# Performance work log

Measured on AMD Instinct MI355X. Metric: run time of the kernel, lower is better.

## Reference

```python
import jax, jax.numpy as jnp
import numpy as np

N_NAMED = 8000   # len(e_dict)
ANON_E = 192     # cfg.anon_e
EMB_DIM = 128    # cfg.emb_dim
N_CLASS = 100
N_REL = 50


def setup_inputs() -> dict:
    key = jax.random.key(0)
    ks = jax.random.split(key, 6)
    s = 1.0 / np.sqrt(EMB_DIM)  # xavier-ish scale
    return {
        "anon_e_emb": jax.random.normal(ks[0], (ANON_E, EMB_DIM), dtype=jnp.float32) * s,
        "e_table": jax.random.normal(ks[1], (N_NAMED, EMB_DIM), dtype=jnp.float32) * s,
        "c_table": jax.random.normal(ks[2], (N_CLASS, EMB_DIM), dtype=jnp.float32) * s,
        "r_table": jax.random.normal(ks[3], (N_REL, EMB_DIM), dtype=jnp.float32) * s,
        "fc0_w": jax.random.normal(ks[4], (1, 2 * EMB_DIM), dtype=jnp.float32) * s,
        "fc0_b": jnp.zeros((1,), dtype=jnp.float32),
        "c_id": 7,
        "r_id": 3,
    }


def reference(anon_e_emb, e_table, c_table, r_table, fc0_w, fc0_b, c_id, r_id):
    """FALCON forward for axiom ObjectSomeValuesFrom(<r> <c>), product t-norm.

    Faithful to _get_c_fs, _get_r_fs, _logical_exist:
      c_fs[j]   = sigmoid(fc_0([c_emb ; e_j]))
      r_fs[i,j] = sigmoid(fc_0([e_i + r_emb ; e_j]))
      out[i]    = max_j r_fs[i,j] * c_fs[j]
    fc_0(cat([l, r])) = l @ w_l + r @ w_r + b  (Linear(2d -> 1)), so the
    [N, N, 2d] concat collapses to two [N] GEMVs plus a broadcast add.
    """
    d = e_table.shape[1]
    e_all = jnp.concatenate([e_table, anon_e_emb], axis=0)  # [N, d]
    w_l = fc0_w[0, :d]   # weights for the left (concat) half
    w_r = fc0_w[0, d:]   # weights for the right half
    b = fc0_b[0]

    c_emb = c_table[c_id]  # [d]
    r_emb = r_table[r_id]  # [d]

    # c_fs: fuzzy membership of every entity in class c  -> [N]
    c_fs = jax.nn.sigmoid(jnp.dot(c_emb, w_l) + e_all @ w_r + b)

    # r_fs[i, j] = sigmoid((e_i + r) . w_l + e_j . w_r + b)  -> [N, N]
    row = (e_all + r_emb) @ w_l  # [N]
    col = e_all @ w_r            # [N]
    r_fs = jax.nn.sigmoid(row[:, None] + col[None, :] + b)

    # _logical_exist with product t-norm: max_j (r_fs * c_fs)
    return jnp.max(r_fs * c_fs[None, :], axis=-1)  # [N]
```

## Files before the change

kernel.cpp:

```cpp
#include <hip/hip_runtime.h>


#define N_NAMED 8000
#define N_ALL   8192
#define D       128
#define K1_BLOCKS (N_ALL / 8)

__global__ __launch_bounds__(256) void k_dots(
    const float* __restrict__ anon_e, const float* __restrict__ e_table,
    const float* __restrict__ fc0_w, float* __restrict__ rowdot,
    float* __restrict__ colmax_part)
{
    const int tid = threadIdx.x;
    const int g   = tid >> 5;
    const int l   = tid & 31;
    const int row = blockIdx.x * 8 + g;

    const float4* rp = (row < N_NAMED)
        ? (const float4*)(e_table + (size_t)row * D)
        : (const float4*)(anon_e + (size_t)(row - N_NAMED) * D);

    float4 e  = rp[l];
    float4 wl = ((const float4*)fc0_w)[l];
    float4 wr = ((const float4*)fc0_w)[32 + l];

    float dl = e.x*wl.x + e.y*wl.y + e.z*wl.z + e.w*wl.w;
    float dr = e.x*wr.x + e.y*wr.y + e.z*wr.z + e.w*wr.w;

    #pragma unroll
    for (int off = 16; off >= 1; off >>= 1) {
        dl += __shfl_xor(dl, off, 64);
        dr += __shfl_xor(dr, off, 64);
    }

    __shared__ float scol[8];
    if (l == 0) { rowdot[row] = dl; scol[g] = dr; }
    __syncthreads();
    if (tid == 0) {
        float m = scol[0];
        #pragma unroll
        for (int i = 1; i < 8; i++) m = fmaxf(m, scol[i]);
        colmax_part[blockIdx.x] = m;
    }
}

__global__ __launch_bounds__(256) void k_final(
    const float* __restrict__ c_table, const float* __restrict__ r_table,
    const float* __restrict__ fc0_w, const float* __restrict__ fc0_b,
    const int* __restrict__ c_id, const int* __restrict__ r_id,
    const float* __restrict__ colmax_part, float* __restrict__ out)
{
    const int tid = threadIdx.x;
    const int i   = blockIdx.x * 256 + tid;

    float m = colmax_part[tid];
    m = fmaxf(m, colmax_part[tid + 256]);
    m = fmaxf(m, colmax_part[tid + 512]);
    m = fmaxf(m, colmax_part[tid + 768]);
    #pragma unroll
    for (int off = 32; off >= 1; off >>= 1)
        m = fmaxf(m, __shfl_xor(m, off, 64));

    __shared__ float swm[4];
    __shared__ float smax;
    if ((tid & 63) == 0) swm[tid >> 6] = m;
    __syncthreads();
    if (tid == 0)
        smax = fmaxf(fmaxf(swm[0], swm[1]), fmaxf(swm[2], swm[3]));
    __syncthreads();
    const float colmax = smax;

    const float b = fc0_b[0];
    const float* cp = c_table + (size_t)c_id[0] * D;
    const float* rp = r_table + (size_t)r_id[0] * D;
    float cw = 0.f, rw = 0.f;
    #pragma unroll 8
    for (int t = 0; t < D; t++) {
        float w = fc0_w[t];
        cw = fmaf(cp[t], w, cw);
        rw = fmaf(rp[t], w, rw);
    }

    float a1 = out[i] + rw + colmax + b;
    float a2 = cw + colmax + b;
    float s1 = 1.f / (1.f + __expf(-a1));
    float s2 = 1.f / (1.f + __expf(-a2));
    out[i] = s1 * s2;
}

extern "C" void kernel_launch(void* const* d_in, const int* in_sizes, int n_in,
                              void* d_out, int out_size, void* d_ws, size_t ws_size,
                              hipStream_t stream) {
    const float* anon_e  = (const float*)d_in[0];
    const float* e_table = (const float*)d_in[1];
    const float* c_table = (const float*)d_in[2];
    const float* r_table = (const float*)d_in[3];
    const float* fc0_w   = (const float*)d_in[4];
    const float* fc0_b   = (const float*)d_in[5];
    const int*   c_id    = (const int*)d_in[6];
    const int*   r_id    = (const int*)d_in[7];
    float* out = (float*)d_out;
    float* ws  = (float*)d_ws;

    k_dots<<<K1_BLOCKS, 256, 0, stream>>>(anon_e, e_table, fc0_w, out, ws);
    k_final<<<N_ALL / 256, 256, 0, stream>>>(c_table, r_table, fc0_w, fc0_b,
                                             c_id, r_id, ws, out);
}
```

Baseline: 75.72 us.

## Fuse dot and finalize kernels into one cooperative kernel with grid sync

Merges the two kernels into a single cooperative launch of 256 blocks, each handling 32 rows. Row dots stay in shared memory instead of a global round trip, and a grid-wide sync replaces the second kernel launch before the column max is reduced. The c/r dot products now use a vectorized warp reduction instead of a serial loop in every thread. The cost is the grid-barrier overhead, and the launch depends on all blocks being co-resident.

```diff
diff --git a/kernel.cpp b/kernel.cpp
--- a/kernel.cpp
+++ b/kernel.cpp
@@ -1,91 +1,92 @@
 #include <hip/hip_runtime.h>
+#include <hip/hip_cooperative_groups.h>
+
+namespace cg = cooperative_groups;
 
 
 #define N_NAMED 8000
 #define N_ALL   8192
 #define D       128
-#define K1_BLOCKS (N_ALL / 8)
+#define NBLK    256
+#define ROWS_PER_BLK (N_ALL / NBLK)
 
-__global__ __launch_bounds__(256) void k_dots(
+__global__ __launch_bounds__(256) void k_fused(
     const float* __restrict__ anon_e, const float* __restrict__ e_table,
-    const float* __restrict__ fc0_w, float* __restrict__ rowdot,
-    float* __restrict__ colmax_part)
+    const float* __restrict__ c_table, const float* __restrict__ r_table,
+    const float* __restrict__ fc0_w, const float* __restrict__ fc0_b,
+    const int* __restrict__ c_id, const int* __restrict__ r_id,
+    float* __restrict__ part, float* __restrict__ out)
 {
     const int tid = threadIdx.x;
     const int g   = tid >> 5;
     const int l   = tid & 31;
-    const int row = blockIdx.x * 8 + g;
 
-    const float4* rp = (row < N_NAMED)
-        ? (const float4*)(e_table + (size_t)row * D)
-        : (const float4*)(anon_e + (size_t)(row - N_NAMED) * D);
+    const float4 wl = ((const float4*)fc0_w)[l];
+    const float4 wr = ((const float4*)fc0_w)[32 + l];
 
-    float4 e  = rp[l];
-    float4 wl = ((const float4*)fc0_w)[l];
-    float4 wr = ((const float4*)fc0_w)[32 + l];
+    __shared__ float sdl[ROWS_PER_BLK];
+    __shared__ float sred[8];
+    __shared__ float swm[4];
+    __shared__ float s_cw, s_rw;
 
-    float dl = e.x*wl.x + e.y*wl.y + e.z*wl.z + e.w*wl.w;
-    float dr = e.x*wr.x + e.y*wr.y + e.z*wr.z + e.w*wr.w;
-
+    float dmax = -3.0e38f;
     #pragma unroll
-    for (int off = 16; off >= 1; off >>= 1) {
-        dl += __shfl_xor(dl, off, 64);
-        dr += __shfl_xor(dr, off, 64);
+    for (int p = 0; p < 4; p++) {
+        const int row = blockIdx.x * ROWS_PER_BLK + p * 8 + g;
+        const float4* rp = (row < N_NAMED)
+            ? (const float4*)(e_table + (size_t)row * D)
+            : (const float4*)(anon_e + (size_t)(row - N_NAMED) * D);
+        float4 e = rp[l];
+        float dl = e.x*wl.x + e.y*wl.y + e.z*wl.z + e.w*wl.w;
+        float dr = e.x*wr.x + e.y*wr.y + e.z*wr.z + e.w*wr.w;
+        #pragma unroll
+        for (int off = 16; off >= 1; off >>= 1) {
+            dl += __shfl_xor(dl, off, 64);
+            dr += __shfl_xor(dr, off, 64);
+        }
+        if (l == 0) sdl[p * 8 + g] = dl;
+        dmax = fmaxf(dmax, dr);
+    }
+    if (l == 0) sred[g] = dmax;
+    __syncthreads();
+    if (tid == 0) {
+        float m = sred[0];
+        #pragma unroll
+        for (int i = 1; i < 8; i++) m = fmaxf(m, sred[i]);
+        part[blockIdx.x] = m;
     }
 
-    __shared__ float scol[8];
-    if (l == 0) { rowdot[row] = dl; scol[g] = dr; }
-    __syncthreads();
-    if (tid == 0) {
-        float m = scol[0];
-        #pragma unroll
-        for (int i = 1; i < 8; i++) m = fmaxf(m, scol[i]);
-        colmax_part[blockIdx.x] = m;
-    }
-}
+    cg::this_grid().sync();
 
-__global__ __launch_bounds__(256) void k_final(
-    const float* __restrict__ c_table, const float* __restrict__ r_table,
-    const float* __restrict__ fc0_w, const float* __restrict__ fc0_b,
-    const int* __restrict__ c_id, const int* __restrict__ r_id,
-    const float* __restrict__ colmax_part, float* __restrict__ out)
-{
-    const int tid = threadIdx.x;
-    const int i   = blockIdx.x * 256 + tid;
-
-    float m = colmax_part[tid];
-    m = fmaxf(m, colmax_part[tid + 256]);
-    m = fmaxf(m, colmax_part[tid + 512]);
-    m = fmaxf(m, colmax_part[tid + 768]);
+    float m = part[tid];
     #pragma unroll
     for (int off = 32; off >= 1; off >>= 1)
         m = fmaxf(m, __shfl_xor(m, off, 64));
+    if ((tid & 63) == 0) swm[tid >> 6] = m;
 
-    __shared__ float swm[4];
-    __shared__ float smax;
-    if ((tid & 63) == 0) swm[tid >> 6] = m;
+    if (tid < 32) {
+        const float4* cp = (const float4*)(c_table + (size_t)c_id[0] * D);
+        const float4* rp = (const float4*)(r_table + (size_t)r_id[0] * D);
+        float4 c4 = cp[l], r4 = rp[l];
+        float cw = c4.x*wl.x + c4.y*wl.y + c4.z*wl.z + c4.w*wl.w;
+        float rw = r4.x*wl.x + r4.y*wl.y + r4.z*wl.z + r4.w*wl.w;
+        #pragma unroll
+        for (int off = 16; off >= 1; off >>= 1) {
+            cw += __shfl_xor(cw, off, 64);
+            rw += __shfl_xor(rw, off, 64);
+        }
+        if (tid == 0) { s_cw = cw; s_rw = rw; }
+    }
     __syncthreads();
-    if (tid == 0)
-        smax = fmaxf(fmaxf(swm[0], swm[1]), fmaxf(swm[2], swm[3]));
-    __syncthreads();
-    const float colmax = smax;
 
-    const float b = fc0_b[0];
-    const float* cp = c_table + (size_t)c_id[0] * D;
-    const float* rp = r_table + (size_t)r_id[0] * D;
-    float cw = 0.f, rw = 0.f;
-    #pragma unroll 8
-    for (int t = 0; t < D; t++) {
-        float w = fc0_w[t];
-        cw = fmaf(cp[t], w, cw);
-        rw = fmaf(rp[t], w, rw);
+    if (tid < ROWS_PER_BLK) {
+        const float colmax = fmaxf(fmaxf(swm[0], swm[1]), fmaxf(swm[2], swm[3]));
+        const float b  = fc0_b[0];
+        const float s2 = 1.f / (1.f + __expf(-(s_cw + colmax + b)));
+        const float a1 = sdl[tid] + s_rw + colmax + b;
+        const float s1 = 1.f / (1.f + __expf(-a1));
+        out[blockIdx.x * ROWS_PER_BLK + tid] = s1 * s2;
     }
-
-    float a1 = out[i] + rw + colmax + b;
-    float a2 = cw + colmax + b;
-    float s1 = 1.f / (1.f + __expf(-a1));
-    float s2 = 1.f / (1.f + __expf(-a2));
-    out[i] = s1 * s2;
 }
 
 extern "C" void kernel_launch(void* const* d_in, const int* in_sizes, int n_in,
@@ -102,7 +103,11 @@
     float* out = (float*)d_out;
     float* ws  = (float*)d_ws;
 
-    k_dots<<<K1_BLOCKS, 256, 0, stream>>>(anon_e, e_table, fc0_w, out, ws);
-    k_final<<<N_ALL / 256, 256, 0, stream>>>(c_table, r_table, fc0_w, fc0_b,
-                                             c_id, r_id, ws, out);
+    void* args[] = {
+        (void*)&anon_e, (void*)&e_table, (void*)&c_table, (void*)&r_table,
+        (void*)&fc0_w,  (void*)&fc0_b,   (void*)&c_id,    (void*)&r_id,
+        (void*)&ws,     (void*)&out
+    };
+    hipLaunchCooperativeKernel((const void*)k_fused, dim3(NBLK), dim3(256),
+                               args, 0, stream);
 }
```

After: 107.8 us. 42.3% more time.
